# Kernel tuning notes

Measured on AMD Instinct MI355X. Metric: run time of the kernel, lower is better.

Reference implementation:

```python
import jax, jax.numpy as jnp
import numpy as np

N, E, F, H, D, C = 50000, 800000, 128, 8, 16, 40


def setup_inputs() -> dict:
    key = jax.random.key(0)
    ks = jax.random.split(key, 12)
    s_in = 1.0 / np.sqrt(F)
    s_h = 1.0 / np.sqrt(H * D)
    return {
        "x": jax.random.normal(ks[0], (N, F), jnp.float32),
        "edge_index": jax.random.randint(ks[1], (2, E), 0, N, jnp.int64),
        "W1": jax.random.normal(ks[2], (F, H * D), jnp.float32) * s_in,
        "a_src1": jax.random.normal(ks[3], (H, D), jnp.float32) * s_h,
        "a_dst1": jax.random.normal(ks[4], (H, D), jnp.float32) * s_h,
        "b1": jnp.zeros((H * D,), jnp.float32),
        "W2": jax.random.normal(ks[5], (H * D, H * D), jnp.float32) * s_h,
        "a_src2": jax.random.normal(ks[6], (H, D), jnp.float32) * s_h,
        "a_dst2": jax.random.normal(ks[7], (H, D), jnp.float32) * s_h,
        "b2": jnp.zeros((H * D,), jnp.float32),
        "Wc": jax.random.normal(ks[8], (H * D, C), jnp.float32) * s_h,
        "bc": jnp.zeros((C,), jnp.float32),
    }


def _gat_layer(x, src, dst, W, a_src, a_dst, b):
    # x: [N, F_in]; src/dst: [E'] (self-loops already appended)
    n = x.shape[0]
    h, d = a_src.shape
    hx = (x @ W).reshape(n, h, d)                      # [N, H, D]
    al_src = jnp.einsum("nhd,hd->nh", hx, a_src)       # [N, H]
    al_dst = jnp.einsum("nhd,hd->nh", hx, a_dst)       # [N, H]
    e = jax.nn.leaky_relu(al_src[src] + al_dst[dst], 0.2)  # [E', H]
    # segment softmax over incoming edges of each destination node
    m = jax.ops.segment_max(e, dst, num_segments=n)    # [N, H]
    e = jnp.exp(e - m[dst])
    z = jax.ops.segment_sum(e, dst, num_segments=n)    # [N, H]
    alpha = e / z[dst]                                 # [E', H]
    out = jax.ops.segment_sum(alpha[:, :, None] * hx[src], dst, num_segments=n)
    return out.reshape(n, h * d) + b


def reference(x, edge_index, W1, a_src1, a_dst1, b1, W2, a_src2, a_dst2, b2, Wc, bc):
    n = x.shape[0]
    loops = jnp.arange(n, dtype=edge_index.dtype)
    src = jnp.concatenate([edge_index[0], loops])  # PyG GATConv adds self-loops
    dst = jnp.concatenate([edge_index[1], loops])
    h = _gat_layer(x, src, dst, W1, a_src1, a_dst1, b1)
    h = jax.nn.elu(h)  # ELU between layers (i < K-1); dropout=None -> no-op
    h = _gat_layer(h, src, dst, W2, a_src2, a_dst2, b2)
    return h @ Wc + bc  # [N, C] logits
```

## Files before the change

kernel.cpp:

```cpp
#include <hip/hip_runtime.h>
#include <hip/hip_bf16.h>
#include <hip/hip_fp16.h>


#define FDIM 128
#define HEADS 8

typedef short bf16x8 __attribute__((ext_vector_type(8)));
typedef float f32x4 __attribute__((ext_vector_type(4)));

typedef __attribute__((address_space(1))) const unsigned gu32;
typedef __attribute__((address_space(3))) unsigned lu32;

__device__ __forceinline__ void load_lds16(const void* g, void* l) {
    __builtin_amdgcn_global_load_lds((gu32*)g, (lu32*)l, 16, 0, 0);
}

__device__ __forceinline__ float leaky02(float x) {
    return fmaxf(x, 0.2f * x);
}

__device__ __forceinline__ unsigned pack2h(float x, float y) {
    __half2 h2 = __floats2half2_rn(x, y);
    return *(unsigned*)&h2;
}

__device__ __forceinline__ void split2(float x, unsigned short& hi, unsigned short& lo) {
    unsigned bits = __float_as_uint(x);
    unsigned h = bits + 0x7fffu + ((bits >> 16) & 1u);
    hi = (unsigned short)(h >> 16);
    float hf = __uint_as_float(h & 0xffff0000u);
    float r = x - hf;
    unsigned rb = __float_as_uint(r);
    unsigned l2 = rb + 0x7fffu + ((rb >> 16) & 1u);
    lo = (unsigned short)(l2 >> 16);
}


__global__ __launch_bounds__(256) void wconv_kernel(const float* __restrict__ W1,
                                                    const float* __restrict__ W2,
                                                    unsigned short* __restrict__ w1_hi,
                                                    unsigned short* __restrict__ w1_lo,
                                                    unsigned short* __restrict__ w2_hi,
                                                    unsigned short* __restrict__ w2_lo) {
    int b = blockIdx.x, t = threadIdx.x;
    const float* W = (b < 16) ? W1 : W2;
    unsigned short* whi = (b < 16) ? w1_hi : w2_hi;
    unsigned short* wlo = (b < 16) ? w1_lo : w2_lo;
    int idx = (b & 15) * 256 + t;
    int k = idx >> 5;
    int c0 = (idx & 31) * 4;
#pragma unroll
    for (int i = 0; i < 4; ++i) {
        int c = c0 + i;
        float v = W[k * FDIM + c];
        unsigned short h, l;
        split2(v, h, l);
        int dest = ((k >> 5) * 8 + (c >> 4)) * 512 +
                   ((c & 15) + (((k >> 3) & 3) << 4)) * 8 + (k & 7);
        whi[dest] = h;
        wlo[dest] = l;
    }
}


__global__ __launch_bounds__(256) void scan_partial(const int* __restrict__ deg,
                                                    int* __restrict__ partials,
                                                    int n) {
    __shared__ int red[256];
    int t = threadIdx.x;
    int base = blockIdx.x * 1024 + t * 4;
    int s = 0;
#pragma unroll
    for (int j = 0; j < 4; ++j) {
        int i = base + j;
        if (i < n) s += deg[i];
    }
    red[t] = s;
    __syncthreads();
    for (int off = 128; off > 0; off >>= 1) {
        if (t < off) red[t] += red[t + off];
        __syncthreads();
    }
    if (t == 0) partials[blockIdx.x] = red[0];
}

__global__ __launch_bounds__(256) void scan_final(const int* __restrict__ deg,
                                                  const int* __restrict__ partials,
                                                  int* __restrict__ row_start,
                                                  int n, int nb) {
    __shared__ int sbuf[256];
    __shared__ int boff_s, total_s;
    int t = threadIdx.x;
    if (t < 64) {
        int carry = 0;
        for (int base = 0; base < nb; base += 64) {
            int idx = base + t;
            int v = (idx < nb) ? partials[idx] : 0;
            int incl = v;
#pragma unroll
            for (int off = 1; off < 64; off <<= 1) {
                int x = __shfl_up(incl, off);
                if (t >= off) incl += x;
            }
            if (idx == (int)blockIdx.x) boff_s = carry + incl - v;
            carry += __shfl(incl, 63);
        }
        if (t == 0) total_s = carry;
    }
    __syncthreads();
    if (blockIdx.x == 0 && t == 0) row_start[n] = total_s;

    int base = blockIdx.x * 1024 + t * 4;
    int v[4];
#pragma unroll
    for (int j = 0; j < 4; ++j) v[j] = (base + j < n) ? deg[base + j] : 0;
    int tsum = v[0] + v[1] + v[2] + v[3];
    sbuf[t] = tsum;
    __syncthreads();
    for (int off = 1; off < 256; off <<= 1) {
        int tmp = (t >= off) ? sbuf[t - off] : 0;
        __syncthreads();
        sbuf[t] += tmp;
        __syncthreads();
    }
    int toff = boff_s + sbuf[t] - tsum;
    int run = 0;
#pragma unroll
    for (int j = 0; j < 4; ++j) {
        int i = base + j;
        if (i < n) row_start[i] = toff + run;
        run += v[j];
    }
}


__global__ __launch_bounds__(256) void scatter_kernel(const int* __restrict__ ei,
                                                      const int* __restrict__ rank,
                                                      const int* __restrict__ row_start,
                                                      int* __restrict__ csr_src,
                                                      int E) {
    int tid = threadIdx.x;
#pragma unroll
    for (int j = 0; j < 4; ++j) {
        int e = blockIdx.x * 1024 + j * 256 + tid;
        if (e < E) {
            int s = ei[e];
            int d = ei[E + e];
            __builtin_nontemporal_store(s, &csr_src[row_start[d] + rank[e]]);
        }
    }
}


template <bool FUSED>
__global__ __launch_bounds__(256, 3) void gemm_mfma(const float* __restrict__ xf,
                                                    const unsigned short* __restrict__ a_hi,
                                                    const unsigned short* __restrict__ a_lo,
                                                    const unsigned short* __restrict__ w_hi,
                                                    const unsigned short* __restrict__ w_lo,
                                                    const float* __restrict__ asrc,
                                                    const float* __restrict__ adst,
                                                    float* __restrict__ als,
                                                    float* __restrict__ ald,
                                                    unsigned* __restrict__ hxf,
                                                    int n,
                                                    const int* __restrict__ ei,
                                                    int* __restrict__ deg,
                                                    int* __restrict__ rank,
                                                    int E, int ng, int grid) {
    __shared__ __align__(16) char smem[49152];
    int tid = threadIdx.x;
    int gb;
    if (FUSED) {
        int bid = blockIdx.x;
        int t0 = (int)((long long)bid * ng / grid);
        int t1 = (int)((long long)(bid + 1) * ng / grid);
        if (t1 == t0) {
            int sb = bid - t0;
#pragma unroll
            for (int j = 0; j < 4; ++j) {
                int e = sb * 1024 + j * 256 + tid;
                if (e < E) rank[e] = atomicAdd(&deg[ei[E + e]], 1);
            }
            return;
        }
        gb = t0;
    } else {
        gb = blockIdx.x;
    }

    int lane = tid & 63;
    int wave = tid >> 6;
    int l15 = lane & 15;
    int lg = lane >> 4;
    int row0 = gb * 32;

    {
#pragma unroll
        for (int c = 0; c < 4; ++c) {
            int s = wave * 4 + c;
            int kc = s >> 2, fr = (s >> 1) & 1, p = s & 1;
            int rg = row0 + fr * 16 + l15;
            if (rg > n - 1) rg = n - 1;
            if (FUSED) {
                load_lds16(xf + (size_t)rg * FDIM + kc * 32 + lg * 8 + p * 4,
                           smem + (size_t)s * 1024);
            } else {
                const unsigned short* src = p ? a_lo : a_hi;
                load_lds16(src + (size_t)rg * FDIM + kc * 32 + lg * 8,
                           smem + (size_t)s * 1024);
            }
        }
    }

    auto stage_B = [&](int kc, int buf) {
#pragma unroll
        for (int c = 0; c < 4; ++c) {
            int s = wave * 4 + c;
            int FC = s >> 1, p = s & 1;
            const unsigned short* src = p ? w_lo : w_hi;
            load_lds16(src + (size_t)(kc * 8 + FC) * 512 + lane * 8,
                       smem + 16384 + (size_t)buf * 16384 + (size_t)(FC * 2 + p) * 1024);
        }
    };
    stage_B(0, 0);
    __syncthreads();

    f32x4 acc[2][2];
#pragma unroll
    for (int fr = 0; fr < 2; ++fr)
#pragma unroll
        for (int fc = 0; fc < 2; ++fc)
#pragma unroll
            for (int r = 0; r < 4; ++r) acc[fr][fc][r] = 0.f;

#pragma unroll
    for (int kc = 0; kc < 4; ++kc) {
        const int cur = kc & 1;
        if (kc < 3) stage_B(kc + 1, cur ^ 1);

        bf16x8 Ah[2], Al[2];
#pragma unroll
        for (int fr = 0; fr < 2; ++fr) {
            if (FUSED) {
                const float4 v0 = *(const float4*)(smem + (size_t)(kc * 4 + fr * 2) * 1024 + lane * 16);
                const float4 v1 = *(const float4*)(smem + (size_t)(kc * 4 + fr * 2 + 1) * 1024 + lane * 16);
                float vv[8] = {v0.x, v0.y, v0.z, v0.w, v1.x, v1.y, v1.z, v1.w};
#pragma unroll
                for (int j = 0; j < 8; ++j) {
                    unsigned bits = __float_as_uint(vv[j]);
                    Ah[fr][j] = (short)(bits >> 16);
                    float hf = __uint_as_float(bits & 0xffff0000u);
                    Al[fr][j] = (short)(__float_as_uint(vv[j] - hf) >> 16);
                }
            } else {
                Ah[fr] = *(const bf16x8*)(smem + (size_t)(kc * 4 + fr * 2) * 1024 + lane * 16);
                Al[fr] = *(const bf16x8*)(smem + (size_t)(kc * 4 + fr * 2 + 1) * 1024 + lane * 16);
            }
        }
        bf16x8 Bh[2], Bl[2];
#pragma unroll
        for (int fc = 0; fc < 2; ++fc) {
            int FC = wave * 2 + fc;
            const char* bb = smem + 16384 + (size_t)cur * 16384 + (size_t)(FC * 2) * 1024;
            Bh[fc] = *(const bf16x8*)(bb + lane * 16);
            Bl[fc] = *(const bf16x8*)(bb + 1024 + lane * 16);
        }
#pragma unroll
        for (int fr = 0; fr < 2; ++fr)
#pragma unroll
            for (int fc = 0; fc < 2; ++fc) {
                acc[fr][fc] = __builtin_amdgcn_mfma_f32_16x16x32_bf16(
                    Al[fr], Bh[fc], acc[fr][fc], 0, 0, 0);
                acc[fr][fc] = __builtin_amdgcn_mfma_f32_16x16x32_bf16(
                    Ah[fr], Bl[fc], acc[fr][fc], 0, 0, 0);
                acc[fr][fc] = __builtin_amdgcn_mfma_f32_16x16x32_bf16(
                    Ah[fr], Bh[fc], acc[fr][fc], 0, 0, 0);
            }
        __syncthreads();
    }

#pragma unroll
    for (int fr = 0; fr < 2; ++fr)
#pragma unroll
        for (int fc = 0; fc < 2; ++fc) {
            int CB = wave * 32 + fc * 16;
            int col = CB + l15;
            float as_ = asrc[col];
            float ad_ = adst[col];
#pragma unroll
            for (int reg = 0; reg < 4; ++reg) {
                int row = row0 + fr * 16 + lg * 4 + reg;
                float v = acc[fr][fc][reg];
                float vn = __shfl_xor(v, 1);
                if ((lane & 1) == 0 && row < n)
                    hxf[(size_t)row * 64 + (col >> 1)] = pack2h(v, vn);
                float ps = v * as_;
                float pd = v * ad_;
                ps += __shfl_xor(ps, 1);
                pd += __shfl_xor(pd, 1);
                ps += __shfl_xor(ps, 2);
                pd += __shfl_xor(pd, 2);
                ps += __shfl_xor(ps, 4);
                pd += __shfl_xor(pd, 4);
                ps += __shfl_xor(ps, 8);
                pd += __shfl_xor(pd, 8);
                if (l15 == 0 && row < n) {
                    als[row * HEADS + (CB >> 4)] = ps;
                    ald[row * HEADS + (CB >> 4)] = pd;
                }
            }
        }
}


__global__ __launch_bounds__(256, 8) void gemm_cls(const unsigned* __restrict__ h_f16,
                                                   const float* __restrict__ W,
                                                   const float* __restrict__ bias,
                                                   float* __restrict__ out,
                                                   int n) {
    __shared__ float xs[32][136];
    __shared__ float ws[32][48];
    int tid = threadIdx.x;
    int row0 = blockIdx.x * 128;
    int lane = tid & 63;
    int wave = tid >> 6;
    int lane2 = lane * 2;
    int wc = wave * 10;

    float acc[2][10];
#pragma unroll
    for (int i = 0; i < 2; ++i)
#pragma unroll
        for (int j = 0; j < 10; ++j) acc[i][j] = 0.f;

    for (int kc = 0; kc < 128; kc += 32) {
        if (kc) __syncthreads();
#pragma unroll
        for (int it = 0; it < 4; ++it) {
            int idx = it * 256 + tid;
            int r = idx >> 3, kg = (idx & 7) * 4;
            float4 v = make_float4(0.f, 0.f, 0.f, 0.f);
            if (row0 + r < n) {
                uint2 hh = *(const uint2*)&h_f16[(size_t)(row0 + r) * 64 + (kc + kg) / 2];
                float2 a = __half22float2(*(__half2*)&hh.x);
                float2 b = __half22float2(*(__half2*)&hh.y);
                v.x = a.x; v.y = a.y; v.z = b.x; v.w = b.y;
            }
            int col = r ^ kg;
            xs[kg + 0][col] = v.x;
            xs[kg + 1][col] = v.y;
            xs[kg + 2][col] = v.z;
            xs[kg + 3][col] = v.w;
        }
#pragma unroll
        for (int it = 0; it < 6; ++it) {
            int idx = it * 256 + tid;
            int kk = idx / 48, c = idx - kk * 48;
            ws[kk][c] = (c < 40) ? W[(size_t)(kc + kk) * 40 + c] : 0.f;
        }
        __syncthreads();
#pragma unroll
        for (int k = 0; k < 32; ++k) {
            int s = ((k >> 2) & 7) << 2;
            float2 av2 = *(const float2*)&xs[k][lane2 ^ s];
            float av[2] = {av2.x, av2.y};
#pragma unroll
            for (int j = 0; j < 10; ++j) {
                float w = ws[k][wc + j];
                acc[0][j] += av[0] * w;
                acc[1][j] += av[1] * w;
            }
        }
    }

#pragma unroll
    for (int i = 0; i < 2; ++i) {
        int row = row0 + lane2 + i;
        if (row < n) {
#pragma unroll
            for (int j = 0; j < 10; ++j)
                out[(size_t)row * 40 + wc + j] = acc[i][j] + bias[wc + j];
        }
    }
}


template <bool DOELU, bool WRITELO>
__global__ __launch_bounds__(256) void gat_aggregate(const unsigned* __restrict__ hxf,
                                                     const float* __restrict__ als,
                                                     const float* __restrict__ ald,
                                                     const int* __restrict__ row_start,
                                                     const int* __restrict__ csr_src,
                                                     const float* __restrict__ bias,
                                                     unsigned* __restrict__ h_hi,
                                                     unsigned* __restrict__ h_lo,
                                                     int n) {
    int wid = threadIdx.x >> 6;
    int lane = threadIdx.x & 63;
    int node = blockIdx.x * 4 + wid;
    if (node >= n) return;

    int rs = row_start[node];
    int deg = row_start[node + 1] - rs;

    int h = lane & 7;
    int hc = lane >> 3;
    int lq = lane >> 3;
    float ald_h = ald[node * HEADS + h];

    float acc0 = 0.f, acc1 = 0.f, zown = 0.f;
    int total = deg + 1;

    int ii = lq;
    int srcv = (ii < deg) ? csr_src[rs + ii] : node;
    float w = (ii < total) ? __expf(leaky02(als[srcv * HEADS + h] + ald_h)) : 0.f;

    int i0 = 0;
    for (; i0 + 8 <= total; i0 += 8) {
        zown += w;
        int ii_n = i0 + 8 + lq;
        int srcv_n = (ii_n < deg) ? csr_src[rs + ii_n] : node;
#pragma unroll
        for (int e = 0; e < 8; ++e) {
            int s = __builtin_amdgcn_readlane(srcv, e * 8);
            float we = __shfl(w, e * 8 + hc);
            unsigned v = hxf[(size_t)s * 64 + lane];
            float2 f = __half22float2(*(__half2*)&v);
            acc0 += we * f.x;
            acc1 += we * f.y;
        }
        float w_n = (ii_n < total) ? __expf(leaky02(als[srcv_n * HEADS + h] + ald_h)) : 0.f;
        srcv = srcv_n;
        w = w_n;
    }
    int rem = total - i0;
    if (rem > 0) {
        zown += w;
        for (int e = 0; e < rem; ++e) {
            int s = __builtin_amdgcn_readlane(srcv, e * 8);
            float we = __shfl(w, e * 8 + hc);
            unsigned v = hxf[(size_t)s * 64 + lane];
            float2 f = __half22float2(*(__half2*)&v);
            acc0 += we * f.x;
            acc1 += we * f.y;
        }
    }

    zown += __shfl_xor(zown, 8);
    zown += __shfl_xor(zown, 16);
    zown += __shfl_xor(zown, 32);
    float z = __shfl(zown, hc);

    float2 bv = *(const float2*)&bias[2 * lane];
    float o0 = acc0 / z + bv.x;
    float o1 = acc1 / z + bv.y;
    if (DOELU) {
        o0 = o0 > 0.f ? o0 : (__expf(o0) - 1.f);
        o1 = o1 > 0.f ? o1 : (__expf(o1) - 1.f);
    }
    if (WRITELO) {
        unsigned short hh0, ll0, hh1, ll1;
        split2(o0, hh0, ll0);
        split2(o1, hh1, ll1);
        h_hi[(size_t)node * 64 + lane] = (unsigned)hh0 | ((unsigned)hh1 << 16);
        h_lo[(size_t)node * 64 + lane] = (unsigned)ll0 | ((unsigned)ll1 << 16);
    } else {
        h_hi[(size_t)node * 64 + lane] = pack2h(o0, o1);
    }
}


extern "C" void kernel_launch(void* const* d_in, const int* in_sizes, int n_in,
                              void* d_out, int out_size, void* d_ws, size_t ws_size,
                              hipStream_t stream) {
    const float* x      = (const float*)d_in[0];
    const int*   ei     = (const int*)d_in[1];
    const float* W1     = (const float*)d_in[2];
    const float* a_src1 = (const float*)d_in[3];
    const float* a_dst1 = (const float*)d_in[4];
    const float* b1     = (const float*)d_in[5];
    const float* W2     = (const float*)d_in[6];
    const float* a_src2 = (const float*)d_in[7];
    const float* a_dst2 = (const float*)d_in[8];
    const float* b2     = (const float*)d_in[9];
    const float* Wc     = (const float*)d_in[10];
    const float* bc     = (const float*)d_in[11];
    float* out = (float*)d_out;

    const int N = in_sizes[0] / FDIM;
    const int E = in_sizes[1] / 2;
    const int NB = (N + 1023) / 1024;

    unsigned* hxf = (unsigned*)d_ws;
    unsigned* xh_u = hxf + (size_t)N * 64;
    unsigned* xl_u = xh_u + (size_t)N * 64;
    float* als  = (float*)(xl_u + (size_t)N * 64);
    float* ald  = als + (size_t)N * HEADS;
    unsigned short* w1_hi = (unsigned short*)(ald + (size_t)N * HEADS);
    unsigned short* w1_lo = w1_hi + 16384;
    unsigned short* w2_hi = w1_lo + 16384;
    unsigned short* w2_lo = w2_hi + 16384;
    int* deg       = (int*)(w2_lo + 16384);
    int* row_start = deg + N;
    int* partials  = row_start + ((N + 8) & ~3);
    int* rank      = partials + ((NB + 4) & ~3);
    int* csr_src   = rank + E;

    hipMemsetAsync(deg, 0, (size_t)N * sizeof(int), stream);
    wconv_kernel<<<32, 256, 0, stream>>>(W1, W2, w1_hi, w1_lo, w2_hi, w2_lo);

    const int ng = (N + 31) / 32;
    const int hb = (E + 1023) / 1024;
    const int grid1 = ng + hb;
    const int agg_grid = (N + 3) / 4;
    const int cls_grid = (N + 127) / 128;

    gemm_mfma<true><<<grid1, 256, 0, stream>>>(x, nullptr, nullptr,
                                               w1_hi, w1_lo,
                                               a_src1, a_dst1, als, ald, hxf, N,
                                               ei, deg, rank, E, ng, grid1);
    scan_partial<<<NB, 256, 0, stream>>>(deg, partials, N);
    scan_final<<<NB, 256, 0, stream>>>(deg, partials, row_start, N, NB);
    scatter_kernel<<<hb, 256, 0, stream>>>(ei, rank, row_start, csr_src, E);

    gat_aggregate<true, true><<<agg_grid, 256, 0, stream>>>(
        hxf, als, ald, row_start, csr_src, b1, xh_u, xl_u, N);
    gemm_mfma<false><<<ng, 256, 0, stream>>>(nullptr,
                                             (const unsigned short*)xh_u,
                                             (const unsigned short*)xl_u,
                                             w2_hi, w2_lo,
                                             a_src2, a_dst2, als, ald, hxf, N,
                                             nullptr, nullptr, nullptr, 0, ng, ng);
    gat_aggregate<false, false><<<agg_grid, 256, 0, stream>>>(
        hxf, als, ald, row_start, csr_src, b2, xh_u, xl_u, N);
    gemm_cls<<<cls_grid, 256, 0, stream>>>(xh_u, Wc, bc, out, N);
}
```

Measured before the change: 217.7 us.

## Make GEMM persistent with register-resident weights and double-buffered A tiles

The MFMA GEMM kernels now launch a fixed 512 blocks that loop over row tiles, instead of one block per 32-row tile. Each block loads its whole hi/lo bf16 weight slice into registers once and prefetches the next A tile into a second LDS buffer while computing the current one. This avoids restaging the weight matrix through LDS for every tile and amortises block launch and prologue cost. The price is many more registers per thread (occupancy bound lowered from 3 to 2) and fewer blocks in flight to hide latency in a kernel that is mostly memory-bound.

```diff
diff --git a/kernel.cpp b/kernel.cpp
--- a/kernel.cpp
+++ b/kernel.cpp
@@ -154,7 +154,7 @@
 
 
 template <bool FUSED>
-__global__ __launch_bounds__(256, 3) void gemm_mfma(const float* __restrict__ xf,
+__global__ __launch_bounds__(256, 2) void gemm_mfma(const float* __restrict__ xf,
                                                     const unsigned short* __restrict__ a_hi,
                                                     const unsigned short* __restrict__ a_lo,
                                                     const unsigned short* __restrict__ w_hi,
@@ -168,14 +168,14 @@
                                                     const int* __restrict__ ei,
                                                     int* __restrict__ deg,
                                                     int* __restrict__ rank,
-                                                    int E, int ng, int grid) {
-    __shared__ __align__(16) char smem[49152];
+                                                    int E, int ng, int ngb, int grid) {
+    __shared__ __align__(16) char smem[32768];
     int tid = threadIdx.x;
     int gb;
     if (FUSED) {
         int bid = blockIdx.x;
-        int t0 = (int)((long long)bid * ng / grid);
-        int t1 = (int)((long long)(bid + 1) * ng / grid);
+        int t0 = (int)((long long)bid * ngb / grid);
+        int t1 = (int)((long long)(bid + 1) * ngb / grid);
         if (t1 == t0) {
             int sb = bid - t0;
 #pragma unroll
@@ -194,124 +194,119 @@
     int wave = tid >> 6;
     int l15 = lane & 15;
     int lg = lane >> 4;
-    int row0 = gb * 32;
-
-    {
+
+    auto stage_A = [&](int tile, int buf) {
 #pragma unroll
         for (int c = 0; c < 4; ++c) {
             int s = wave * 4 + c;
             int kc = s >> 2, fr = (s >> 1) & 1, p = s & 1;
-            int rg = row0 + fr * 16 + l15;
+            int rg = tile * 32 + fr * 16 + l15;
             if (rg > n - 1) rg = n - 1;
             if (FUSED) {
                 load_lds16(xf + (size_t)rg * FDIM + kc * 32 + lg * 8 + p * 4,
-                           smem + (size_t)s * 1024);
+                           smem + (size_t)buf * 16384 + (size_t)s * 1024);
             } else {
                 const unsigned short* src = p ? a_lo : a_hi;
                 load_lds16(src + (size_t)rg * FDIM + kc * 32 + lg * 8,
-                           smem + (size_t)s * 1024);
-            }
-        }
-    }
-
-    auto stage_B = [&](int kc, int buf) {
-#pragma unroll
-        for (int c = 0; c < 4; ++c) {
-            int s = wave * 4 + c;
-            int FC = s >> 1, p = s & 1;
-            const unsigned short* src = p ? w_lo : w_hi;
-            load_lds16(src + (size_t)(kc * 8 + FC) * 512 + lane * 8,
-                       smem + 16384 + (size_t)buf * 16384 + (size_t)(FC * 2 + p) * 1024);
+                           smem + (size_t)buf * 16384 + (size_t)s * 1024);
+            }
         }
     };
-    stage_B(0, 0);
-    __syncthreads();
-
-    f32x4 acc[2][2];
-#pragma unroll
-    for (int fr = 0; fr < 2; ++fr)
-#pragma unroll
-        for (int fc = 0; fc < 2; ++fc)
-#pragma unroll
-            for (int r = 0; r < 4; ++r) acc[fr][fc][r] = 0.f;
-
-#pragma unroll
-    for (int kc = 0; kc < 4; ++kc) {
-        const int cur = kc & 1;
-        if (kc < 3) stage_B(kc + 1, cur ^ 1);
-
-        bf16x8 Ah[2], Al[2];
-#pragma unroll
-        for (int fr = 0; fr < 2; ++fr) {
-            if (FUSED) {
-                const float4 v0 = *(const float4*)(smem + (size_t)(kc * 4 + fr * 2) * 1024 + lane * 16);
-                const float4 v1 = *(const float4*)(smem + (size_t)(kc * 4 + fr * 2 + 1) * 1024 + lane * 16);
-                float vv[8] = {v0.x, v0.y, v0.z, v0.w, v1.x, v1.y, v1.z, v1.w};
-#pragma unroll
-                for (int j = 0; j < 8; ++j) {
-                    unsigned bits = __float_as_uint(vv[j]);
-                    Ah[fr][j] = (short)(bits >> 16);
-                    float hf = __uint_as_float(bits & 0xffff0000u);
-                    Al[fr][j] = (short)(__float_as_uint(vv[j] - hf) >> 16);
+
+    stage_A(gb, 0);
+
+    bf16x8 BH[4][2], BL[4][2];
+#pragma unroll
+    for (int kc = 0; kc < 4; ++kc)
+#pragma unroll
+        for (int fc = 0; fc < 2; ++fc) {
+            size_t off = (size_t)(kc * 8 + wave * 2 + fc) * 512 + lane * 8;
+            BH[kc][fc] = *(const bf16x8*)(w_hi + off);
+            BL[kc][fc] = *(const bf16x8*)(w_lo + off);
+        }
+
+    int buf = 0;
+    for (int tile = gb; tile < ng; tile += ngb, buf ^= 1) {
+        __syncthreads();
+        if (tile + ngb < ng) stage_A(tile + ngb, buf ^ 1);
+        int row0 = tile * 32;
+
+        f32x4 acc[2][2];
+#pragma unroll
+        for (int fr = 0; fr < 2; ++fr)
+#pragma unroll
+            for (int fc = 0; fc < 2; ++fc)
+#pragma unroll
+                for (int r = 0; r < 4; ++r) acc[fr][fc][r] = 0.f;
+
+#pragma unroll
+        for (int kc = 0; kc < 4; ++kc) {
+            bf16x8 Ah[2], Al[2];
+#pragma unroll
+            for (int fr = 0; fr < 2; ++fr) {
+                const char* base = smem + (size_t)buf * 16384 +
+                                   (size_t)(kc * 4 + fr * 2) * 1024;
+                if (FUSED) {
+                    const float4 v0 = *(const float4*)(base + lane * 16);
+                    const float4 v1 = *(const float4*)(base + 1024 + lane * 16);
+                    float vv[8] = {v0.x, v0.y, v0.z, v0.w, v1.x, v1.y, v1.z, v1.w};
+#pragma unroll
+                    for (int j = 0; j < 8; ++j) {
+                        unsigned bits = __float_as_uint(vv[j]);
+                        Ah[fr][j] = (short)(bits >> 16);
+                        float hf = __uint_as_float(bits & 0xffff0000u);
+                        Al[fr][j] = (short)(__float_as_uint(vv[j] - hf) >> 16);
+                    }
+                } else {
+                    Ah[fr] = *(const bf16x8*)(base + lane * 16);
+                    Al[fr] = *(const bf16x8*)(base + 1024 + lane * 16);
                 }
-            } else {
-                Ah[fr] = *(const bf16x8*)(smem + (size_t)(kc * 4 + fr * 2) * 1024 + lane * 16);
-                Al[fr] = *(const bf16x8*)(smem + (size_t)(kc * 4 + fr * 2 + 1) * 1024 + lane * 16);
-            }
-        }
-        bf16x8 Bh[2], Bl[2];
-#pragma unroll
-        for (int fc = 0; fc < 2; ++fc) {
-            int FC = wave * 2 + fc;
-            const char* bb = smem + 16384 + (size_t)cur * 16384 + (size_t)(FC * 2) * 1024;
-            Bh[fc] = *(const bf16x8*)(bb + lane * 16);
-            Bl[fc] = *(const bf16x8*)(bb + 1024 + lane * 16);
-        }
+            }
+#pragma unroll
+            for (int fr = 0; fr < 2; ++fr)
+#pragma unroll
+                for (int fc = 0; fc < 2; ++fc) {
+                    acc[fr][fc] = __builtin_amdgcn_mfma_f32_16x16x32_bf16(
+                        Al[fr], BH[kc][fc], acc[fr][fc], 0, 0, 0);
+                    acc[fr][fc] = __builtin_amdgcn_mfma_f32_16x16x32_bf16(
+                        Ah[fr], BL[kc][fc], acc[fr][fc], 0, 0, 0);
+                    acc[fr][fc] = __builtin_amdgcn_mfma_f32_16x16x32_bf16(
+                        Ah[fr], BH[kc][fc], acc[fr][fc], 0, 0, 0);
+                }
+        }
+
 #pragma unroll
         for (int fr = 0; fr < 2; ++fr)
 #pragma unroll
             for (int fc = 0; fc < 2; ++fc) {
-                acc[fr][fc] = __builtin_amdgcn_mfma_f32_16x16x32_bf16(
-                    Al[fr], Bh[fc], acc[fr][fc], 0, 0, 0);
-                acc[fr][fc] = __builtin_amdgcn_mfma_f32_16x16x32_bf16(
-                    Ah[fr], Bl[fc], acc[fr][fc], 0, 0, 0);
-                acc[fr][fc] = __builtin_amdgcn_mfma_f32_16x16x32_bf16(
-                    Ah[fr], Bh[fc], acc[fr][fc], 0, 0, 0);
-            }
-        __syncthreads();
-    }
-
-#pragma unroll
-    for (int fr = 0; fr < 2; ++fr)
-#pragma unroll
-        for (int fc = 0; fc < 2; ++fc) {
-            int CB = wave * 32 + fc * 16;
-            int col = CB + l15;
-            float as_ = asrc[col];
-            float ad_ = adst[col];
-#pragma unroll
-            for (int reg = 0; reg < 4; ++reg) {
-                int row = row0 + fr * 16 + lg * 4 + reg;
-                float v = acc[fr][fc][reg];
-                float vn = __shfl_xor(v, 1);
-                if ((lane & 1) == 0 && row < n)
-                    hxf[(size_t)row * 64 + (col >> 1)] = pack2h(v, vn);
-                float ps = v * as_;
-                float pd = v * ad_;
-                ps += __shfl_xor(ps, 1);
-                pd += __shfl_xor(pd, 1);
-                ps += __shfl_xor(ps, 2);
-                pd += __shfl_xor(pd, 2);
-                ps += __shfl_xor(ps, 4);
-                pd += __shfl_xor(pd, 4);
-                ps += __shfl_xor(ps, 8);
-                pd += __shfl_xor(pd, 8);
-                if (l15 == 0 && row < n) {
-                    als[row * HEADS + (CB >> 4)] = ps;
-                    ald[row * HEADS + (CB >> 4)] = pd;
+                int CB = wave * 32 + fc * 16;
+                int col = CB + l15;
+                float as_ = asrc[col];
+                float ad_ = adst[col];
+#pragma unroll
+                for (int reg = 0; reg < 4; ++reg) {
+                    int row = row0 + fr * 16 + lg * 4 + reg;
+                    float v = acc[fr][fc][reg];
+                    float vn = __shfl_xor(v, 1);
+                    if ((lane & 1) == 0 && row < n)
+                        hxf[(size_t)row * 64 + (col >> 1)] = pack2h(v, vn);
+                    float ps = v * as_;
+                    float pd = v * ad_;
+                    ps += __shfl_xor(ps, 1);
+                    pd += __shfl_xor(pd, 1);
+                    ps += __shfl_xor(ps, 2);
+                    pd += __shfl_xor(pd, 2);
+                    ps += __shfl_xor(ps, 4);
+                    pd += __shfl_xor(pd, 4);
+                    ps += __shfl_xor(ps, 8);
+                    pd += __shfl_xor(pd, 8);
+                    if (l15 == 0 && row < n) {
+                        als[row * HEADS + (CB >> 4)] = ps;
+                        ald[row * HEADS + (CB >> 4)] = pd;
+                    }
                 }
             }
-        }
+    }
 }
 
 
@@ -511,28 +506,30 @@
     hipMemsetAsync(deg, 0, (size_t)N * sizeof(int), stream);
     wconv_kernel<<<32, 256, 0, stream>>>(W1, W2, w1_hi, w1_lo, w2_hi, w2_lo);
 
-    const int ng = (N + 31) / 32;
-    const int hb = (E + 1023) / 1024;
-    const int grid1 = ng + hb;
+    const int ng  = (N + 31) / 32;
+    const int ngb = 512;
+    const int hb  = (E + 1023) / 1024;
+    const int grid1 = ngb + hb;
     const int agg_grid = (N + 3) / 4;
     const int cls_grid = (N + 127) / 128;
 
     gemm_mfma<true><<<grid1, 256, 0, stream>>>(x, nullptr, nullptr,
                                                w1_hi, w1_lo,
                                                a_src1, a_dst1, als, ald, hxf, N,
-                                               ei, deg, rank, E, ng, grid1);
+                                               ei, deg, rank, E, ng, ngb, grid1);
     scan_partial<<<NB, 256, 0, stream>>>(deg, partials, N);
     scan_final<<<NB, 256, 0, stream>>>(deg, partials, row_start, N, NB);
     scatter_kernel<<<hb, 256, 0, stream>>>(ei, rank, row_start, csr_src, E);
 
     gat_aggregate<true, true><<<agg_grid, 256, 0, stream>>>(
         hxf, als, ald, row_start, csr_src, b1, xh_u, xl_u, N);
-    gemm_mfma<false><<<ng, 256, 0, stream>>>(nullptr,
-                                             (const unsigned short*)xh_u,
-                                             (const unsigned short*)xl_u,
-                                             w2_hi, w2_lo,
-                                             a_src2, a_dst2, als, ald, hxf, N,
-                                             nullptr, nullptr, nullptr, 0, ng, ng);
+    gemm_mfma<false><<<ngb, 256, 0, stream>>>(nullptr,
+                                              (const unsigned short*)xh_u,
+                                              (const unsigned short*)xl_u,
+                                              w2_hi, w2_lo,
+                                              a_src2, a_dst2, als, ald, hxf, N,
+                                              nullptr, nullptr, nullptr, 0,
+                                              ng, ngb, ngb);
     gat_aggregate<false, false><<<agg_grid, 256, 0, stream>>>(
         hxf, als, ald, row_start, csr_src, b2, xh_u, xl_u, N);
     gemm_cls<<<cls_grid, 256, 0, stream>>>(xh_u, Wc, bc, out, N);
```

New measurement: 224.9 us. +3.3%, slower.
